# Performance work log

Hardware: AMD Instinct MI355X
Metric: run time of the kernel (lower is better)

Reference implementation:

```python
import jax, jax.numpy as jnp
import numpy as np

N = 100000   # num nodes
D = 128      # node_emb_dim
R = 8        # num_relations
E = 1600000  # num edges


def setup_inputs() -> dict:
    key = jax.random.key(0)
    k0, k1, k2, k3, k4 = jax.random.split(key, 5)
    x = jax.random.normal(k0, (N, D), dtype=jnp.float32)
    edge_index = jax.random.randint(k1, (2, E), 0, N, dtype=jnp.int32)
    edge_type = jax.random.randint(k2, (E,), 0, R, dtype=jnp.int32)
    scale = 1.0 / np.sqrt(D)
    W = (jax.random.normal(k3, (R, D, D), dtype=jnp.float32) * scale)       # per-relation weight
    W_root = (jax.random.normal(k4, (D, D), dtype=jnp.float32) * scale)     # root (self-loop) weight
    bias = jnp.zeros((D,), dtype=jnp.float32)
    return {"x": x, "W": W, "W_root": W_root, "bias": bias,
            "edge_index": edge_index, "edge_type": edge_type}


def reference(x, W, W_root, bias, edge_index, edge_type):
    # PyG RGCNConv (num_bases=None, aggr='mean', root_weight=True, bias=True):
    # out_i = x_i @ W_root + bias + sum_r mean_{j in N_r(i)} x_j @ W_r
    # Mean aggregation is linear, so aggregate neighbor features per (node, relation)
    # first, then apply the per-relation transform (avoids [E,D,D] intermediates).
    src, dst = edge_index[0], edge_index[1]
    seg = dst * R + edge_type                                   # [E] segment id per (dst, rel)
    cnt = jax.ops.segment_sum(jnp.ones((E,), x.dtype), seg, num_segments=N * R)  # [N*R]
    sums = jax.ops.segment_sum(x[src], seg, num_segments=N * R)                   # [N*R, D]
    mean = sums / jnp.maximum(cnt, 1.0)[:, None]                                  # [N*R, D]
    rel_out = jnp.einsum('nrd,rde->ne', mean.reshape(N, R, D), W)                 # [N, D]
    return rel_out + x @ W_root + bias
```

## Files before the change

kernel.cpp:

```cpp
#include <hip/hip_runtime.h>


constexpr int D = 128;
constexpr int R = 8;
constexpr int CW = 64;
constexpr int LDA = 40;
constexpr int TILE2 = 4096;
constexpr int CAP = 3072;
constexpr int MAXRUNS = 8192;
constexpr int TCH = 32;

typedef __bf16 bf16x8 __attribute__((ext_vector_type(8)));
typedef float  f32x4  __attribute__((ext_vector_type(4)));
typedef unsigned short u16x8 __attribute__((ext_vector_type(8)));
typedef unsigned short u16x4 __attribute__((ext_vector_type(4)));

__device__ __forceinline__ unsigned short f2bf(float f) {
    unsigned u = __builtin_bit_cast(unsigned, f);
    u += 0x7FFFu + ((u >> 16) & 1u);
    return (unsigned short)(u >> 16);
}
__device__ __forceinline__ float bf2f(unsigned short h) {
    return __builtin_bit_cast(float, (unsigned)h << 16);
}

__global__ __launch_bounds__(256)
void xbf_kernel(const float* __restrict__ x, unsigned short* __restrict__ xbf, int nquad) {
    int stride = gridDim.x * 256;
    for (int i = blockIdx.x * 256 + threadIdx.x; i < nquad; i += stride) {
        float4 v = ((const float4*)x)[i];
        u16x4 o;
        o[0] = f2bf(v.x); o[1] = f2bf(v.y); o[2] = f2bf(v.z); o[3] = f2bf(v.w);
        ((u16x4*)xbf)[i] = o;
    }
}

__global__ __launch_bounds__(256)
void count_kernel(const int* __restrict__ dst, const int* __restrict__ et,
                  int* __restrict__ counts, int E, int nruns) {
    __shared__ int lh[MAXRUNS];
    for (int i = threadIdx.x; i < nruns; i += 256) lh[i] = 0;
    __syncthreads();
    int t0 = blockIdx.x * TILE2;
    #pragma unroll 4
    for (int j = 0; j < TILE2 / 256; ++j) {
        int e = t0 + j * 256 + threadIdx.x;
        if (e < E) {
            int seg = dst[e] * R + et[e];
            atomicAdd(&lh[seg >> 7], 1);
        }
    }
    __syncthreads();
    int* row = counts + (size_t)blockIdx.x * nruns;
    for (int i = threadIdx.x; i < nruns; i += 256) row[i] = lh[i];
}

__global__ __launch_bounds__(256)
void colscanA_kernel(const int* __restrict__ counts, int* __restrict__ part,
                     int ntiles, int nruns, int cpt) {
    int r = blockIdx.x * 256 + threadIdx.x;
    int c = blockIdx.y;
    if (r >= nruns) return;
    int t0 = c * cpt, t1 = min(t0 + cpt, ntiles);
    int acc = 0;
    for (int t = t0; t < t1; ++t) acc += counts[(size_t)t * nruns + r];
    part[(size_t)c * nruns + r] = acc;
}

__global__ __launch_bounds__(256)
void colscanB_kernel(int* __restrict__ part, int* __restrict__ runtot,
                     int nchunks, int nruns) {
    int r = blockIdx.x * 256 + threadIdx.x;
    if (r >= nruns) return;
    int acc = 0;
    for (int c = 0; c < nchunks; ++c) {
        size_t i = (size_t)c * nruns + r;
        int v = part[i];
        part[i] = acc;
        acc += v;
    }
    runtot[r] = acc;
}

__global__ __launch_bounds__(256)
void colscanC_kernel(int* __restrict__ counts, const int* __restrict__ part,
                     int ntiles, int nruns, int cpt) {
    int r = blockIdx.x * 256 + threadIdx.x;
    int c = blockIdx.y;
    if (r >= nruns) return;
    int t0 = c * cpt, t1 = min(t0 + cpt, ntiles);
    int acc = part[(size_t)c * nruns + r];
    for (int t = t0; t < t1; ++t) {
        size_t i = (size_t)t * nruns + r;
        int v = counts[i];
        counts[i] = acc;
        acc += v;
    }
}

__global__ __launch_bounds__(64)
void runscan_kernel(const int* __restrict__ runtot, int* __restrict__ runbase, int nb) {
    int lane = threadIdx.x;
    int carry = 0;
    for (int base = 0; base < nb; base += 64) {
        int i = base + lane;
        int orig = (i < nb) ? runtot[i] : 0;
        int v = orig;
        #pragma unroll
        for (int off = 1; off < 64; off <<= 1) {
            int u = __shfl_up(v, off, 64);
            if (lane >= off) v += u;
        }
        int tot = __shfl(v, 63, 64);
        if (i < nb) runbase[i] = carry + (v - orig);
        carry += tot;
    }
    if (lane == 0) runbase[nb] = carry;
}

__global__ __launch_bounds__(256)
void place_kernel(const int* __restrict__ src, const int* __restrict__ dst,
                  const int* __restrict__ et, const int* __restrict__ counts,
                  const int* __restrict__ runbase, unsigned* __restrict__ epack,
                  int E, int nruns) {
    __shared__ int lh[MAXRUNS];
    for (int i = threadIdx.x; i < nruns; i += 256) lh[i] = 0;
    __syncthreads();
    int t0 = blockIdx.x * TILE2;
    const int* colpre = counts + (size_t)blockIdx.x * nruns;
    #pragma unroll 4
    for (int j = 0; j < TILE2 / 256; ++j) {
        int e = t0 + j * 256 + threadIdx.x;
        if (e < E) {
            int seg  = dst[e] * R + et[e];
            int run  = seg >> 7;
            int rank = atomicAdd(&lh[run], 1);
            int pos  = runbase[run] + colpre[run] + rank;
            epack[pos] = (unsigned)src[e] | ((unsigned)(seg & 127) << 24);
        }
    }
}

__global__ __launch_bounds__(256)
void aggregate_kernel(const unsigned short* __restrict__ xbf,
                      const unsigned* __restrict__ epack,
                      const int* __restrict__ runbase,
                      unsigned short* __restrict__ mean,
                      int nseg, int c0) {
    __shared__ unsigned raw[CAP];
    __shared__ unsigned srt[CAP];
    __shared__ int hist[128], sc[128], offs[128], cur[128];

    const int tid  = threadIdx.x;
    const int run  = blockIdx.x;
    const int base = runbase[run];
    const int size = runbase[run + 1] - base;
    const int c8   = tid & 7;
    const int sg0  = tid >> 3;

    float a[4][8] = {};
    int   cacc[4] = {};

    const int nchunks = (size + CAP - 1) / CAP;
    for (int ch = 0; ch < nchunks; ++ch) {
        int off = ch * CAP;
        int n   = min(CAP, size - off);

        if (tid < 128) hist[tid] = 0;
        __syncthreads();
        for (int j = tid; j < n; j += 256) {
            unsigned e = epack[base + off + j];
            raw[j] = e;
            atomicAdd(&hist[e >> 24], 1);
        }
        __syncthreads();
        if (tid < 128) sc[tid] = hist[tid];
        __syncthreads();
        for (int o = 1; o < 128; o <<= 1) {
            int u = 0;
            if (tid < 128 && tid >= o) u = sc[tid - o];
            __syncthreads();
            if (tid < 128) sc[tid] += u;
            __syncthreads();
        }
        if (tid < 128) { int x0 = sc[tid] - hist[tid]; offs[tid] = x0; cur[tid] = x0; }
        __syncthreads();
        for (int j = tid; j < n; j += 256) {
            unsigned e = raw[j];
            int r = atomicAdd(&cur[e >> 24], 1);
            srt[r] = e;
        }
        __syncthreads();
        #pragma unroll
        for (int i = 0; i < 4; ++i) {
            int s  = sg0 + i * 32;
            int st = offs[s], cn = hist[s];
            cacc[i] += cn;
            for (int k = 0; k < cn; k += 4) {
                unsigned e0 = srt[st + k];
                int s1ok = (k + 1 < cn), s2ok = (k + 2 < cn), s3ok = (k + 3 < cn);
                unsigned e1 = s1ok ? srt[st + k + 1] : 0;
                unsigned e2 = s2ok ? srt[st + k + 2] : 0;
                unsigned e3 = s3ok ? srt[st + k + 3] : 0;
                u16x8 v0 = *(const u16x8*)(xbf + ((size_t)(e0 & 0xFFFFFF) << 7) + c0 + c8 * 8);
                #pragma unroll
                for (int q = 0; q < 8; ++q) a[i][q] += bf2f(v0[q]);
                if (s1ok) {
                    u16x8 v = *(const u16x8*)(xbf + ((size_t)(e1 & 0xFFFFFF) << 7) + c0 + c8 * 8);
                    #pragma unroll
                    for (int q = 0; q < 8; ++q) a[i][q] += bf2f(v[q]);
                }
                if (s2ok) {
                    u16x8 v = *(const u16x8*)(xbf + ((size_t)(e2 & 0xFFFFFF) << 7) + c0 + c8 * 8);
                    #pragma unroll
                    for (int q = 0; q < 8; ++q) a[i][q] += bf2f(v[q]);
                }
                if (s3ok) {
                    u16x8 v = *(const u16x8*)(xbf + ((size_t)(e3 & 0xFFFFFF) << 7) + c0 + c8 * 8);
                    #pragma unroll
                    for (int q = 0; q < 8; ++q) a[i][q] += bf2f(v[q]);
                }
            }
        }
        __syncthreads();
    }

    #pragma unroll
    for (int i = 0; i < 4; ++i) {
        int seg = run * 128 + sg0 + i * 32;
        if (seg < nseg) {
            float inv = (cacc[i] > 0) ? 1.0f / (float)cacc[i] : 0.0f;
            u16x8 o;
            #pragma unroll
            for (int q = 0; q < 8; ++q) o[q] = f2bf(a[i][q] * inv);
            *(u16x8*)(mean + ((size_t)seg << 6) + c8 * 8) = o;
        }
    }
}

__global__ __launch_bounds__(256)
void wallt_kernel(const float* __restrict__ Wroot, const float* __restrict__ W,
                  unsigned short* __restrict__ WallTc) {
    int idx = blockIdx.x * 256 + threadIdx.x;
    if (idx >= 128 * 1152) return;
    int n = idx / 1152, k = idx % 1152;
    float v = (k < 1024) ? W[(size_t)(k >> 7) * 16384 + (size_t)(k & 127) * 128 + n]
                         : Wroot[(size_t)(k - 1024) * 128 + n];
    WallTc[idx] = f2bf(v);
}

template<bool FIRST>
__global__ __launch_bounds__(256)
void mfma_gemm_kernel(const unsigned short* __restrict__ xbf,
                      const unsigned short* __restrict__ mean,
                      const unsigned short* __restrict__ WallTc,
                      const float* __restrict__ bias,
                      float* __restrict__ out,
                      int N, int c0) {
    constexpr int NT = FIRST ? 20 : 16;
    __shared__ unsigned short As[64 * LDA];
    __shared__ unsigned short Bs[128 * LDA];
    const int tid  = threadIdx.x;
    const int nd0  = blockIdx.x * 64;
    const int lane = tid & 63;
    const int wid  = tid >> 6;
    const int wm   = wid >> 1;
    const int wn   = wid & 1;
    const int arow = tid >> 2;
    const int aoct = tid & 3;
    const int brow = tid >> 1;
    const int bhalf = tid & 1;

    f32x4 acc[2][4] = {};

    const int  anode = nd0 + arow;
    const bool aok   = anode < N;

    for (int kt = 0; kt < NT; ++kt) {
        if (kt) __syncthreads();
        u16x8 av8;
        #pragma unroll
        for (int j = 0; j < 8; ++j) av8[j] = 0;
        int kbase;
        if (FIRST && kt < 4) {
            if (aok)
                av8 = *(const u16x8*)(xbf + ((size_t)anode << 7) + kt * 32 + aoct * 8);
            kbase = 1024 + kt * 32;
        } else {
            int lk = (kt - (FIRST ? 4 : 0)) * 32;
            if (aok)
                av8 = *(const u16x8*)(mean + ((size_t)anode << 9) + lk + aoct * 8);
            kbase = (lk >> 6) * 128 + c0 + (lk & 63);
        }
        const u16x8* wp = (const u16x8*)(WallTc + (size_t)brow * 1152 + kbase + bhalf * 16);
        u16x8 b0 = wp[0], b1 = wp[1];

        *(u16x8*)&As[arow * LDA + aoct * 8]       = av8;
        *(u16x8*)&Bs[brow * LDA + bhalf * 16]     = b0;
        *(u16x8*)&Bs[brow * LDA + bhalf * 16 + 8] = b1;
        __syncthreads();

        const int ko = (lane >> 4) * 8;
        const int rl = lane & 15;
        bf16x8 af[2], bf[4];
        #pragma unroll
        for (int f = 0; f < 2; ++f)
            af[f] = __builtin_bit_cast(bf16x8,
                *(const u16x8*)&As[(wm * 32 + f * 16 + rl) * LDA + ko]);
        #pragma unroll
        for (int f = 0; f < 4; ++f)
            bf[f] = __builtin_bit_cast(bf16x8,
                *(const u16x8*)&Bs[(wn * 64 + f * 16 + rl) * LDA + ko]);
        #pragma unroll
        for (int mf = 0; mf < 2; ++mf)
            #pragma unroll
            for (int nf = 0; nf < 4; ++nf)
                acc[mf][nf] = __builtin_amdgcn_mfma_f32_16x16x32_bf16(af[mf], bf[nf],
                                                                     acc[mf][nf], 0, 0, 0);
    }

    const int rl = lane & 15;
    const int rg = lane >> 4;
    #pragma unroll
    for (int nf = 0; nf < 4; ++nf) {
        int n = wn * 64 + nf * 16 + rl;
        float bb = FIRST ? bias[n] : 0.0f;
        #pragma unroll
        for (int mf = 0; mf < 2; ++mf) {
            #pragma unroll
            for (int i = 0; i < 4; ++i) {
                int nd = nd0 + wm * 32 + mf * 16 + rg * 4 + i;
                if (nd < N) {
                    size_t o = (size_t)nd * 128 + n;
                    if (FIRST) out[o] = acc[mf][nf][i] + bb;
                    else       out[o] += acc[mf][nf][i];
                }
            }
        }
    }
}

extern "C" void kernel_launch(void* const* d_in, const int* in_sizes, int n_in,
                              void* d_out, int out_size, void* d_ws, size_t ws_size,
                              hipStream_t stream) {
    const float* x     = (const float*)d_in[0];
    const float* W     = (const float*)d_in[1];
    const float* Wroot = (const float*)d_in[2];
    const float* bias  = (const float*)d_in[3];
    const int*   ei    = (const int*)d_in[4];
    const int*   et    = (const int*)d_in[5];
    float*       out   = (float*)d_out;

    const int N = in_sizes[0] / D;
    const int E = in_sizes[5];
    const int* src = ei;
    const int* dst = ei + E;

    const int NSEG   = N * R;
    const int NRUNS  = (NSEG + 127) / 128;
    const int NTILES = (E + TILE2 - 1) / TILE2;
    if (NRUNS > MAXRUNS) return;

    const size_t mean_bytes   = (size_t)NSEG * CW * 2;
    const size_t xbf_bytes    = (size_t)N * D * 2;
    const size_t walltc_bytes = (size_t)128 * 1152 * 2;
    const size_t counts_bytes = (size_t)NTILES * NRUNS * 4;
    const size_t part_bytes   = (size_t)TCH * NRUNS * 4;
    const size_t need = mean_bytes + xbf_bytes + walltc_bytes + counts_bytes +
                        part_bytes + ((size_t)NRUNS + (NRUNS + 1) + E) * 4 + 256;
    if (ws_size < need) return;

    char* p = (char*)d_ws;
    unsigned short* mean   = (unsigned short*)p;  p += mean_bytes;
    unsigned short* xbf    = (unsigned short*)p;  p += xbf_bytes;
    unsigned short* WallTc = (unsigned short*)p;  p += walltc_bytes;
    int*      counts  = (int*)p;       p += counts_bytes;
    int*      part    = (int*)p;       p += part_bytes;
    int*      runtot  = (int*)p;       p += (size_t)NRUNS * 4;
    int*      runbase = (int*)p;       p += (size_t)(NRUNS + 1) * 4;
    unsigned* epack   = (unsigned*)p;

    xbf_kernel<<<1024, 256, 0, stream>>>(x, xbf, N * D / 4);
    wallt_kernel<<<(128 * 1152 + 255) / 256, 256, 0, stream>>>(Wroot, W, WallTc);

    count_kernel<<<NTILES, 256, 0, stream>>>(dst, et, counts, E, NRUNS);

    const int cpt = (NTILES + TCH - 1) / TCH;
    dim3 cgrid((NRUNS + 255) / 256, TCH);
    colscanA_kernel<<<cgrid, 256, 0, stream>>>(counts, part, NTILES, NRUNS, cpt);
    colscanB_kernel<<<(NRUNS + 255) / 256, 256, 0, stream>>>(part, runtot, TCH, NRUNS);
    colscanC_kernel<<<cgrid, 256, 0, stream>>>(counts, part, NTILES, NRUNS, cpt);
    runscan_kernel<<<1, 64, 0, stream>>>(runtot, runbase, NRUNS);

    place_kernel<<<NTILES, 256, 0, stream>>>(src, dst, et, counts, runbase, epack, E, NRUNS);

    const int gx = (N + 63) / 64;
    for (int c = 0; c < 2; ++c) {
        int c0 = c * CW;
        aggregate_kernel<<<NRUNS, 256, 0, stream>>>(xbf, epack, runbase, mean, NSEG, c0);
        if (c == 0)
            mfma_gemm_kernel<true><<<gx, 256, 0, stream>>>(
                xbf, mean, WallTc, bias, out, N, c0);
        else
            mfma_gemm_kernel<false><<<gx, 256, 0, stream>>>(
                xbf, mean, WallTc, bias, out, N, c0);
    }
}
```

Measured before the change: 372.4 us.

## Aggregate all feature columns in one pass when workspace allows full-width mean

When the workspace can hold a full 128-column mean buffer, the aggregation runs once over all columns with 16 threads per segment, and a single GEMM consumes the full K range. This replaces the two-pass column-split scheme, so the edge list is scanned once instead of twice and one aggregate and one GEMM launch are dropped, along with the read-modify-write of the output. Per-tile counts are also narrowed to 16-bit to cut traffic in the count/scan/place stages, and mean stores become nontemporal. The cost is twice the mean buffer size and fewer segments per thread with more gather parallelism per segment. The 16-bit counts would overflow if a tile held more than 65535 edges for one run, which cannot happen with a tile size of 4096.

New measurement: 372.9 us. Within noise of the previous version (+0.1%).

```diff
diff --git a/kernel.cpp b/kernel.cpp
--- a/kernel.cpp
+++ b/kernel.cpp
@@ -3,7 +3,6 @@
 
 constexpr int D = 128;
 constexpr int R = 8;
-constexpr int CW = 64;
 constexpr int LDA = 40;
 constexpr int TILE2 = 4096;
 constexpr int CAP = 3072;
@@ -37,7 +36,7 @@
 
 __global__ __launch_bounds__(256)
 void count_kernel(const int* __restrict__ dst, const int* __restrict__ et,
-                  int* __restrict__ counts, int E, int nruns) {
+                  unsigned short* __restrict__ counts, int E, int nruns) {
     __shared__ int lh[MAXRUNS];
     for (int i = threadIdx.x; i < nruns; i += 256) lh[i] = 0;
     __syncthreads();
@@ -51,12 +50,12 @@
         }
     }
     __syncthreads();
-    int* row = counts + (size_t)blockIdx.x * nruns;
-    for (int i = threadIdx.x; i < nruns; i += 256) row[i] = lh[i];
-}
-
-__global__ __launch_bounds__(256)
-void colscanA_kernel(const int* __restrict__ counts, int* __restrict__ part,
+    unsigned short* row = counts + (size_t)blockIdx.x * nruns;
+    for (int i = threadIdx.x; i < nruns; i += 256) row[i] = (unsigned short)lh[i];
+}
+
+__global__ __launch_bounds__(256)
+void colscanA_kernel(const unsigned short* __restrict__ counts, int* __restrict__ part,
                      int ntiles, int nruns, int cpt) {
     int r = blockIdx.x * 256 + threadIdx.x;
     int c = blockIdx.y;
@@ -83,7 +82,7 @@
 }
 
 __global__ __launch_bounds__(256)
-void colscanC_kernel(int* __restrict__ counts, const int* __restrict__ part,
+void colscanC_kernel(unsigned short* __restrict__ counts, const int* __restrict__ part,
                      int ntiles, int nruns, int cpt) {
     int r = blockIdx.x * 256 + threadIdx.x;
     int c = blockIdx.y;
@@ -93,7 +92,7 @@
     for (int t = t0; t < t1; ++t) {
         size_t i = (size_t)t * nruns + r;
         int v = counts[i];
-        counts[i] = acc;
+        counts[i] = (unsigned short)acc;
         acc += v;
     }
 }
@@ -120,14 +119,14 @@
 
 __global__ __launch_bounds__(256)
 void place_kernel(const int* __restrict__ src, const int* __restrict__ dst,
-                  const int* __restrict__ et, const int* __restrict__ counts,
+                  const int* __restrict__ et, const unsigned short* __restrict__ counts,
                   const int* __restrict__ runbase, unsigned* __restrict__ epack,
                   int E, int nruns) {
     __shared__ int lh[MAXRUNS];
     for (int i = threadIdx.x; i < nruns; i += 256) lh[i] = 0;
     __syncthreads();
     int t0 = blockIdx.x * TILE2;
-    const int* colpre = counts + (size_t)blockIdx.x * nruns;
+    const unsigned short* colpre = counts + (size_t)blockIdx.x * nruns;
     #pragma unroll 4
     for (int j = 0; j < TILE2 / 256; ++j) {
         int e = t0 + j * 256 + threadIdx.x;
@@ -135,18 +134,21 @@
             int seg  = dst[e] * R + et[e];
             int run  = seg >> 7;
             int rank = atomicAdd(&lh[run], 1);
-            int pos  = runbase[run] + colpre[run] + rank;
+            int pos  = runbase[run] + (int)colpre[run] + rank;
             epack[pos] = (unsigned)src[e] | ((unsigned)(seg & 127) << 24);
         }
     }
 }
 
+template<int NOCT>
 __global__ __launch_bounds__(256)
 void aggregate_kernel(const unsigned short* __restrict__ xbf,
                       const unsigned* __restrict__ epack,
                       const int* __restrict__ runbase,
                       unsigned short* __restrict__ mean,
                       int nseg, int c0) {
+    constexpr int GROUPS = 256 / NOCT;
+    constexpr int SPT    = 128 / GROUPS;
     __shared__ unsigned raw[CAP];
     __shared__ unsigned srt[CAP];
     __shared__ int hist[128], sc[128], offs[128], cur[128];
@@ -155,11 +157,11 @@
     const int run  = blockIdx.x;
     const int base = runbase[run];
     const int size = runbase[run + 1] - base;
-    const int c8   = tid & 7;
-    const int sg0  = tid >> 3;
-
-    float a[4][8] = {};
-    int   cacc[4] = {};
+    const int c8   = tid & (NOCT - 1);
+    const int sg0  = tid / NOCT;
+
+    float a[SPT][8] = {};
+    int   cacc[SPT] = {};
 
     const int nchunks = (size + CAP - 1) / CAP;
     for (int ch = 0; ch < nchunks; ++ch) {
@@ -192,8 +194,8 @@
         }
         __syncthreads();
         #pragma unroll
-        for (int i = 0; i < 4; ++i) {
-            int s  = sg0 + i * 32;
+        for (int i = 0; i < SPT; ++i) {
+            int s  = sg0 + i * GROUPS;
             int st = offs[s], cn = hist[s];
             cacc[i] += cn;
             for (int k = 0; k < cn; k += 4) {
@@ -226,14 +228,15 @@
     }
 
     #pragma unroll
-    for (int i = 0; i < 4; ++i) {
-        int seg = run * 128 + sg0 + i * 32;
+    for (int i = 0; i < SPT; ++i) {
+        int seg = run * 128 + sg0 + i * GROUPS;
         if (seg < nseg) {
             float inv = (cacc[i] > 0) ? 1.0f / (float)cacc[i] : 0.0f;
             u16x8 o;
             #pragma unroll
             for (int q = 0; q < 8; ++q) o[q] = f2bf(a[i][q] * inv);
-            *(u16x8*)(mean + ((size_t)seg << 6) + c8 * 8) = o;
+            __builtin_nontemporal_store(o,
+                (u16x8*)(mean + (size_t)seg * (NOCT * 8) + c8 * 8));
         }
     }
 }
@@ -249,7 +252,7 @@
     WallTc[idx] = f2bf(v);
 }
 
-template<bool FIRST>
+template<int MODE>
 __global__ __launch_bounds__(256)
 void mfma_gemm_kernel(const unsigned short* __restrict__ xbf,
                       const unsigned short* __restrict__ mean,
@@ -257,7 +260,8 @@
                       const float* __restrict__ bias,
                       float* __restrict__ out,
                       int N, int c0) {
-    constexpr int NT = FIRST ? 20 : 16;
+    constexpr int  NT      = (MODE == 0) ? 36 : (MODE == 1 ? 20 : 16);
+    constexpr bool HASROOT = (MODE <= 1);
     __shared__ unsigned short As[64 * LDA];
     __shared__ unsigned short Bs[128 * LDA];
     const int tid  = threadIdx.x;
@@ -282,15 +286,21 @@
         #pragma unroll
         for (int j = 0; j < 8; ++j) av8[j] = 0;
         int kbase;
-        if (FIRST && kt < 4) {
+        if (HASROOT && kt < 4) {
             if (aok)
                 av8 = *(const u16x8*)(xbf + ((size_t)anode << 7) + kt * 32 + aoct * 8);
             kbase = 1024 + kt * 32;
         } else {
-            int lk = (kt - (FIRST ? 4 : 0)) * 32;
-            if (aok)
-                av8 = *(const u16x8*)(mean + ((size_t)anode << 9) + lk + aoct * 8);
-            kbase = (lk >> 6) * 128 + c0 + (lk & 63);
+            int lk = (kt - (HASROOT ? 4 : 0)) * 32;
+            if (MODE == 0) {
+                if (aok)
+                    av8 = *(const u16x8*)(mean + ((size_t)anode << 10) + lk + aoct * 8);
+                kbase = lk;
+            } else {
+                if (aok)
+                    av8 = *(const u16x8*)(mean + ((size_t)anode << 9) + lk + aoct * 8);
+                kbase = (lk >> 6) * 128 + c0 + (lk & 63);
+            }
         }
         const u16x8* wp = (const u16x8*)(WallTc + (size_t)brow * 1152 + kbase + bhalf * 16);
         u16x8 b0 = wp[0], b1 = wp[1];
@@ -324,7 +334,7 @@
     #pragma unroll
     for (int nf = 0; nf < 4; ++nf) {
         int n = wn * 64 + nf * 16 + rl;
-        float bb = FIRST ? bias[n] : 0.0f;
+        float bb = (MODE <= 1) ? bias[n] : 0.0f;
         #pragma unroll
         for (int mf = 0; mf < 2; ++mf) {
             #pragma unroll
@@ -332,8 +342,8 @@
                 int nd = nd0 + wm * 32 + mf * 16 + rg * 4 + i;
                 if (nd < N) {
                     size_t o = (size_t)nd * 128 + n;
-                    if (FIRST) out[o] = acc[mf][nf][i] + bb;
-                    else       out[o] += acc[mf][nf][i];
+                    if (MODE <= 1) out[o] = acc[mf][nf][i] + bb;
+                    else           out[o] += acc[mf][nf][i];
                 }
             }
         }
@@ -361,20 +371,25 @@
     const int NTILES = (E + TILE2 - 1) / TILE2;
     if (NRUNS > MAXRUNS) return;
 
-    const size_t mean_bytes   = (size_t)NSEG * CW * 2;
     const size_t xbf_bytes    = (size_t)N * D * 2;
     const size_t walltc_bytes = (size_t)128 * 1152 * 2;
-    const size_t counts_bytes = (size_t)NTILES * NRUNS * 4;
+    const size_t counts_bytes = (size_t)NTILES * NRUNS * 2;
     const size_t part_bytes   = (size_t)TCH * NRUNS * 4;
-    const size_t need = mean_bytes + xbf_bytes + walltc_bytes + counts_bytes +
-                        part_bytes + ((size_t)NRUNS + (NRUNS + 1) + E) * 4 + 256;
-    if (ws_size < need) return;
+    const size_t tail_bytes   = counts_bytes + part_bytes +
+                                ((size_t)NRUNS + (NRUNS + 1) + E) * 4 + 512;
+
+    const size_t need128 = (size_t)NSEG * 128 * 2 + xbf_bytes + walltc_bytes + tail_bytes;
+    const size_t need64  = (size_t)NSEG * 64  * 2 + xbf_bytes + walltc_bytes + tail_bytes;
+    bool single = (need128 <= ws_size);
+    if (!single && need64 > ws_size) return;
+
+    const size_t mean_bytes = single ? (size_t)NSEG * 128 * 2 : (size_t)NSEG * 64 * 2;
 
     char* p = (char*)d_ws;
     unsigned short* mean   = (unsigned short*)p;  p += mean_bytes;
     unsigned short* xbf    = (unsigned short*)p;  p += xbf_bytes;
     unsigned short* WallTc = (unsigned short*)p;  p += walltc_bytes;
-    int*      counts  = (int*)p;       p += counts_bytes;
+    unsigned short* counts = (unsigned short*)p;  p += counts_bytes;
     int*      part    = (int*)p;       p += part_bytes;
     int*      runtot  = (int*)p;       p += (size_t)NRUNS * 4;
     int*      runbase = (int*)p;       p += (size_t)(NRUNS + 1) * 4;
@@ -395,14 +410,17 @@
     place_kernel<<<NTILES, 256, 0, stream>>>(src, dst, et, counts, runbase, epack, E, NRUNS);
 
     const int gx = (N + 63) / 64;
-    for (int c = 0; c < 2; ++c) {
-        int c0 = c * CW;
-        aggregate_kernel<<<NRUNS, 256, 0, stream>>>(xbf, epack, runbase, mean, NSEG, c0);
-        if (c == 0)
-            mfma_gemm_kernel<true><<<gx, 256, 0, stream>>>(
-                xbf, mean, WallTc, bias, out, N, c0);
-        else
-            mfma_gemm_kernel<false><<<gx, 256, 0, stream>>>(
-                xbf, mean, WallTc, bias, out, N, c0);
-    }
-}
+    if (single) {
+        aggregate_kernel<16><<<NRUNS, 256, 0, stream>>>(xbf, epack, runbase, mean, NSEG, 0);
+        mfma_gemm_kernel<0><<<gx, 256, 0, stream>>>(xbf, mean, WallTc, bias, out, N, 0);
+    } else {
+        for (int c = 0; c < 2; ++c) {
+            int c0 = c * 64;
+            aggregate_kernel<8><<<NRUNS, 256, 0, stream>>>(xbf, epack, runbase, mean, NSEG, c0);
+            if (c == 0)
+                mfma_gemm_kernel<1><<<gx, 256, 0, stream>>>(xbf, mean, WallTc, bias, out, N, c0);
+            else
+                mfma_gemm_kernel<2><<<gx, 256, 0, stream>>>(xbf, mean, WallTc, bias, out, N, c0);
+        }
+    }
+}
```

## Fuse prep kernels, shrink tile counts to u16, and use a single GEMM pass

Applied to the files above, without the earlier changes.

Merges the bf16 conversion of x, the per-tile edge counting and the weight transpose into one launch that dispatches on block index, removing two kernel launches. Per-tile run counts are stored as 16-bit values, halving that buffer's traffic in the column scans and the place step. The two aggregation halves now write separate mean buffers, so one GEMM with K=1152 replaces two GEMM passes. This drops the read-modify-write of the output in the second pass. The cost is extra workspace for the second mean buffer and a wider workspace bound.

New measurement: 364.4 us. -2.1%, faster.

```diff
diff --git a/kernel.cpp b/kernel.cpp
--- a/kernel.cpp
+++ b/kernel.cpp
@@ -3,7 +3,6 @@
 
 constexpr int D = 128;
 constexpr int R = 8;
-constexpr int CW = 64;
 constexpr int LDA = 40;
 constexpr int TILE2 = 4096;
 constexpr int CAP = 3072;
@@ -24,39 +23,55 @@
     return __builtin_bit_cast(float, (unsigned)h << 16);
 }
 
-__global__ __launch_bounds__(256)
-void xbf_kernel(const float* __restrict__ x, unsigned short* __restrict__ xbf, int nquad) {
-    int stride = gridDim.x * 256;
-    for (int i = blockIdx.x * 256 + threadIdx.x; i < nquad; i += stride) {
-        float4 v = ((const float4*)x)[i];
-        u16x4 o;
-        o[0] = f2bf(v.x); o[1] = f2bf(v.y); o[2] = f2bf(v.z); o[3] = f2bf(v.w);
-        ((u16x4*)xbf)[i] = o;
-    }
-}
-
-__global__ __launch_bounds__(256)
-void count_kernel(const int* __restrict__ dst, const int* __restrict__ et,
-                  int* __restrict__ counts, int E, int nruns) {
+constexpr int XB = 640;
+constexpr int WB = 64;
+__global__ __launch_bounds__(256)
+void prep_kernel(const float* __restrict__ x, unsigned short* __restrict__ xbf,
+                 int nquad,
+                 const int* __restrict__ dst, const int* __restrict__ et,
+                 unsigned short* __restrict__ counts, int E, int nruns, int ntiles,
+                 const float* __restrict__ Wroot, const float* __restrict__ W,
+                 unsigned short* __restrict__ WallTc) {
     __shared__ int lh[MAXRUNS];
-    for (int i = threadIdx.x; i < nruns; i += 256) lh[i] = 0;
-    __syncthreads();
-    int t0 = blockIdx.x * TILE2;
-    #pragma unroll 4
-    for (int j = 0; j < TILE2 / 256; ++j) {
-        int e = t0 + j * 256 + threadIdx.x;
-        if (e < E) {
-            int seg = dst[e] * R + et[e];
-            atomicAdd(&lh[seg >> 7], 1);
-        }
-    }
-    __syncthreads();
-    int* row = counts + (size_t)blockIdx.x * nruns;
-    for (int i = threadIdx.x; i < nruns; i += 256) row[i] = lh[i];
-}
-
-__global__ __launch_bounds__(256)
-void colscanA_kernel(const int* __restrict__ counts, int* __restrict__ part,
+    if (blockIdx.x < XB) {
+        int stride = XB * 256;
+        for (int i = blockIdx.x * 256 + threadIdx.x; i < nquad; i += stride) {
+            float4 v = ((const float4*)x)[i];
+            u16x4 o;
+            o[0] = f2bf(v.x); o[1] = f2bf(v.y); o[2] = f2bf(v.z); o[3] = f2bf(v.w);
+            ((u16x4*)xbf)[i] = o;
+        }
+    } else if (blockIdx.x < XB + (unsigned)ntiles) {
+        int tile = blockIdx.x - XB;
+        for (int i = threadIdx.x; i < nruns; i += 256) lh[i] = 0;
+        __syncthreads();
+        int t0 = tile * TILE2;
+        #pragma unroll 4
+        for (int j = 0; j < TILE2 / 256; ++j) {
+            int e = t0 + j * 256 + threadIdx.x;
+            if (e < E) {
+                int seg = dst[e] * R + et[e];
+                atomicAdd(&lh[seg >> 7], 1);
+            }
+        }
+        __syncthreads();
+        unsigned short* row = counts + (size_t)tile * nruns;
+        for (int i = threadIdx.x; i < nruns; i += 256) row[i] = (unsigned short)lh[i];
+    } else {
+        int b = blockIdx.x - XB - ntiles;
+        int stride = WB * 256;
+        for (int idx = b * 256 + threadIdx.x; idx < 128 * 1152; idx += stride) {
+            int n = idx / 1152, k = idx % 1152;
+            float v = (k < 1024)
+                ? W[(size_t)(k >> 7) * 16384 + (size_t)(k & 127) * 128 + n]
+                : Wroot[(size_t)(k - 1024) * 128 + n];
+            WallTc[idx] = f2bf(v);
+        }
+    }
+}
+
+__global__ __launch_bounds__(256)
+void colscanA_kernel(const unsigned short* __restrict__ counts, int* __restrict__ part,
                      int ntiles, int nruns, int cpt) {
     int r = blockIdx.x * 256 + threadIdx.x;
     int c = blockIdx.y;
@@ -83,7 +98,7 @@
 }
 
 __global__ __launch_bounds__(256)
-void colscanC_kernel(int* __restrict__ counts, const int* __restrict__ part,
+void colscanC_kernel(unsigned short* __restrict__ counts, const int* __restrict__ part,
                      int ntiles, int nruns, int cpt) {
     int r = blockIdx.x * 256 + threadIdx.x;
     int c = blockIdx.y;
@@ -93,7 +108,7 @@
     for (int t = t0; t < t1; ++t) {
         size_t i = (size_t)t * nruns + r;
         int v = counts[i];
-        counts[i] = acc;
+        counts[i] = (unsigned short)acc;
         acc += v;
     }
 }
@@ -120,14 +135,14 @@
 
 __global__ __launch_bounds__(256)
 void place_kernel(const int* __restrict__ src, const int* __restrict__ dst,
-                  const int* __restrict__ et, const int* __restrict__ counts,
+                  const int* __restrict__ et, const unsigned short* __restrict__ counts,
                   const int* __restrict__ runbase, unsigned* __restrict__ epack,
                   int E, int nruns) {
     __shared__ int lh[MAXRUNS];
     for (int i = threadIdx.x; i < nruns; i += 256) lh[i] = 0;
     __syncthreads();
     int t0 = blockIdx.x * TILE2;
-    const int* colpre = counts + (size_t)blockIdx.x * nruns;
+    const unsigned short* colpre = counts + (size_t)blockIdx.x * nruns;
     #pragma unroll 4
     for (int j = 0; j < TILE2 / 256; ++j) {
         int e = t0 + j * 256 + threadIdx.x;
@@ -135,7 +150,7 @@
             int seg  = dst[e] * R + et[e];
             int run  = seg >> 7;
             int rank = atomicAdd(&lh[run], 1);
-            int pos  = runbase[run] + colpre[run] + rank;
+            int pos  = runbase[run] + (int)colpre[run] + rank;
             epack[pos] = (unsigned)src[e] | ((unsigned)(seg & 127) << 24);
         }
     }
@@ -239,25 +254,13 @@
 }
 
 __global__ __launch_bounds__(256)
-void wallt_kernel(const float* __restrict__ Wroot, const float* __restrict__ W,
-                  unsigned short* __restrict__ WallTc) {
-    int idx = blockIdx.x * 256 + threadIdx.x;
-    if (idx >= 128 * 1152) return;
-    int n = idx / 1152, k = idx % 1152;
-    float v = (k < 1024) ? W[(size_t)(k >> 7) * 16384 + (size_t)(k & 127) * 128 + n]
-                         : Wroot[(size_t)(k - 1024) * 128 + n];
-    WallTc[idx] = f2bf(v);
-}
-
-template<bool FIRST>
-__global__ __launch_bounds__(256)
 void mfma_gemm_kernel(const unsigned short* __restrict__ xbf,
-                      const unsigned short* __restrict__ mean,
+                      const unsigned short* __restrict__ mean0,
+                      const unsigned short* __restrict__ mean1,
                       const unsigned short* __restrict__ WallTc,
                       const float* __restrict__ bias,
-                      float* __restrict__ out,
-                      int N, int c0) {
-    constexpr int NT = FIRST ? 20 : 16;
+                      float* __restrict__ out, int N) {
+    constexpr int NT = 36;
     __shared__ unsigned short As[64 * LDA];
     __shared__ unsigned short Bs[128 * LDA];
     const int tid  = threadIdx.x;
@@ -282,15 +285,19 @@
         #pragma unroll
         for (int j = 0; j < 8; ++j) av8[j] = 0;
         int kbase;
-        if (FIRST && kt < 4) {
+        if (kt < 4) {
             if (aok)
                 av8 = *(const u16x8*)(xbf + ((size_t)anode << 7) + kt * 32 + aoct * 8);
             kbase = 1024 + kt * 32;
         } else {
-            int lk = (kt - (FIRST ? 4 : 0)) * 32;
+            int lk = (kt - 4) * 32;
+            int r  = lk >> 7;
+            int c  = lk & 127;
+            const unsigned short* mbuf = (c & 64) ? mean1 : mean0;
             if (aok)
-                av8 = *(const u16x8*)(mean + ((size_t)anode << 9) + lk + aoct * 8);
-            kbase = (lk >> 6) * 128 + c0 + (lk & 63);
+                av8 = *(const u16x8*)(mbuf + (((size_t)anode * 8 + r) << 6)
+                                      + (c & 63) + aoct * 8);
+            kbase = lk;
         }
         const u16x8* wp = (const u16x8*)(WallTc + (size_t)brow * 1152 + kbase + bhalf * 16);
         u16x8 b0 = wp[0], b1 = wp[1];
@@ -324,17 +331,13 @@
     #pragma unroll
     for (int nf = 0; nf < 4; ++nf) {
         int n = wn * 64 + nf * 16 + rl;
-        float bb = FIRST ? bias[n] : 0.0f;
+        float bb = bias[n];
         #pragma unroll
         for (int mf = 0; mf < 2; ++mf) {
             #pragma unroll
             for (int i = 0; i < 4; ++i) {
                 int nd = nd0 + wm * 32 + mf * 16 + rg * 4 + i;
-                if (nd < N) {
-                    size_t o = (size_t)nd * 128 + n;
-                    if (FIRST) out[o] = acc[mf][nf][i] + bb;
-                    else       out[o] += acc[mf][nf][i];
-                }
+                if (nd < N) out[(size_t)nd * 128 + n] = acc[mf][nf][i] + bb;
             }
         }
     }
@@ -361,29 +364,28 @@
     const int NTILES = (E + TILE2 - 1) / TILE2;
     if (NRUNS > MAXRUNS) return;
 
-    const size_t mean_bytes   = (size_t)NSEG * CW * 2;
+    const size_t mean_half    = (size_t)NSEG * 64 * 2;
     const size_t xbf_bytes    = (size_t)N * D * 2;
     const size_t walltc_bytes = (size_t)128 * 1152 * 2;
-    const size_t counts_bytes = (size_t)NTILES * NRUNS * 4;
+    const size_t counts_bytes = (size_t)NTILES * NRUNS * 2;
     const size_t part_bytes   = (size_t)TCH * NRUNS * 4;
-    const size_t need = mean_bytes + xbf_bytes + walltc_bytes + counts_bytes +
-                        part_bytes + ((size_t)NRUNS + (NRUNS + 1) + E) * 4 + 256;
+    const size_t need = 2 * mean_half + xbf_bytes + walltc_bytes + counts_bytes +
+                        part_bytes + ((size_t)NRUNS + (NRUNS + 1) + E) * 4 + 512;
     if (ws_size < need) return;
 
     char* p = (char*)d_ws;
-    unsigned short* mean   = (unsigned short*)p;  p += mean_bytes;
+    unsigned short* mean0  = (unsigned short*)p;  p += mean_half;
+    unsigned short* mean1  = (unsigned short*)p;  p += mean_half;
     unsigned short* xbf    = (unsigned short*)p;  p += xbf_bytes;
     unsigned short* WallTc = (unsigned short*)p;  p += walltc_bytes;
-    int*      counts  = (int*)p;       p += counts_bytes;
+    unsigned short* counts = (unsigned short*)p;  p += counts_bytes;
     int*      part    = (int*)p;       p += part_bytes;
     int*      runtot  = (int*)p;       p += (size_t)NRUNS * 4;
     int*      runbase = (int*)p;       p += (size_t)(NRUNS + 1) * 4;
     unsigned* epack   = (unsigned*)p;
 
-    xbf_kernel<<<1024, 256, 0, stream>>>(x, xbf, N * D / 4);
-    wallt_kernel<<<(128 * 1152 + 255) / 256, 256, 0, stream>>>(Wroot, W, WallTc);
-
-    count_kernel<<<NTILES, 256, 0, stream>>>(dst, et, counts, E, NRUNS);
+    prep_kernel<<<XB + NTILES + WB, 256, 0, stream>>>(
+        x, xbf, N * D / 4, dst, et, counts, E, NRUNS, NTILES, Wroot, W, WallTc);
 
     const int cpt = (NTILES + TCH - 1) / TCH;
     dim3 cgrid((NRUNS + 255) / 256, TCH);
@@ -394,15 +396,9 @@
 
     place_kernel<<<NTILES, 256, 0, stream>>>(src, dst, et, counts, runbase, epack, E, NRUNS);
 
+    aggregate_kernel<<<NRUNS, 256, 0, stream>>>(xbf, epack, runbase, mean0, NSEG, 0);
+    aggregate_kernel<<<NRUNS, 256, 0, stream>>>(xbf, epack, runbase, mean1, NSEG, 64);
+
     const int gx = (N + 63) / 64;
-    for (int c = 0; c < 2; ++c) {
-        int c0 = c * CW;
-        aggregate_kernel<<<NRUNS, 256, 0, stream>>>(xbf, epack, runbase, mean, NSEG, c0);
-        if (c == 0)
-            mfma_gemm_kernel<true><<<gx, 256, 0, stream>>>(
-                xbf, mean, WallTc, bias, out, N, c0);
-        else
-            mfma_gemm_kernel<false><<<gx, 256, 0, stream>>>(
-                xbf, mean, WallTc, bias, out, N, c0);
-    }
-}
+    mfma_gemm_kernel<<<gx, 256, 0, stream>>>(xbf, mean0, mean1, WallTc, bias, out, N);
+}
```
